# Performance work log

Measured on AMD Instinct MI355X. Metric: run time of the kernel, lower is better.

## Reference

```python
import jax, jax.numpy as jnp
import numpy as np
import math

N = 100000
D = 128       # input_dim
DK = 32       # d_k
H = 4         # heads
DV = D // H   # d_v = 32
DFF = 512     # 4 * input_dim
EPS = 1e-5


def layer_norm(x, g, b):
    mu = jnp.mean(x, axis=-1, keepdims=True)
    var = jnp.var(x, axis=-1, keepdims=True)
    return (x - mu) * jax.lax.rsqrt(var + EPS) * g + b


def setup_inputs() -> dict:
    key = jax.random.key(0)
    ks = jax.random.split(key, 10)
    x = jax.random.normal(ks[0], (N, D), dtype=jnp.float32)
    neighbor_index = jax.random.randint(ks[1], (N, 4), 0, N)
    # xavier-ish scaled params
    w_q = jax.random.normal(ks[2], (H, D, DK), dtype=jnp.float32) * math.sqrt(2.0 / (D + DK))
    w_k = jax.random.normal(ks[3], (H, 5, D, DK), dtype=jnp.float32) * math.sqrt(2.0 / (D + DK))
    w_v = jax.random.normal(ks[4], (H, 5, D, DV), dtype=jnp.float32) * math.sqrt(2.0 / (D + DV))
    W1 = jax.random.normal(ks[5], (D, DFF), dtype=jnp.float32) * math.sqrt(1.0 / D)
    b1 = jnp.zeros((DFF,), dtype=jnp.float32)
    W2 = jax.random.normal(ks[6], (DFF, D), dtype=jnp.float32) * math.sqrt(1.0 / DFF)
    b2 = jnp.zeros((D,), dtype=jnp.float32)
    g1 = jnp.ones((D,), dtype=jnp.float32)
    beta1 = jnp.zeros((D,), dtype=jnp.float32)
    g2 = jnp.ones((D,), dtype=jnp.float32)
    beta2 = jnp.zeros((D,), dtype=jnp.float32)
    return {"x": x, "neighbor_index": neighbor_index, "w_q": w_q, "w_k": w_k,
            "w_v": w_v, "W1": W1, "b1": b1, "W2": W2, "b2": b2,
            "g1": g1, "beta1": beta1, "g2": g2, "beta2": beta2}


def attention(x, neighbor_index, w_q, w_k, w_v):
    # gather the 4 typed neighbors and prepend the self node -> (N, 5, D)
    x_nb = jnp.concatenate([x[:, None, :], x[neighbor_index]], axis=1)
    Q = jnp.einsum('nd,hdk->hnk', x, w_q)                 # (H, N, DK)
    K = jnp.einsum('nrd,hrdk->hnrk', x_nb, w_k)           # (H, N, 5, DK)
    V = jnp.einsum('nrd,hrdv->hnrv', x_nb, w_v)           # (H, N, 5, DV)
    A = jnp.einsum('hnk,hnrk->hnr', Q, K) / math.sqrt(DK)
    # NOTE: original torch code applies softmax over dim=1 (the node axis),
    # reproduced faithfully here.
    A = jax.nn.softmax(A, axis=1)
    Z = jnp.einsum('hnr,hnrv->hnv', A, V)                 # (H, N, DV)
    return jnp.transpose(Z, (1, 0, 2)).reshape(x.shape[0], -1)  # (N, H*DV)


def reference(x, neighbor_index, w_q, w_k, w_v, W1, b1, W2, b2, g1, beta1, g2, beta2):
    attn = attention(x, neighbor_index, w_q, w_k, w_v)
    h = layer_norm(x + attn, g1, beta1)
    ffn = jax.nn.relu(h @ W1 + b1) @ W2 + b2
    return layer_norm(h + ffn, g2, beta2)
```

## Files before the change

kernel.cpp:

```cpp
#include <hip/hip_runtime.h>
#include <hip/hip_bf16.h>

typedef unsigned short u16;
typedef __attribute__((ext_vector_type(8))) short short8;
typedef __attribute__((ext_vector_type(4))) float f32x4;
typedef __attribute__((ext_vector_type(4))) float float4v;
typedef __attribute__((ext_vector_type(4))) unsigned short us4;
typedef __attribute__((ext_vector_type(4))) int int4v;

#define NN       100000
#define OFF_WK   16384
#define OFF_WV   98304
#define OFF_W1   180224
#define PACK_ELEMS 311296

#define WS_LWS   0u
#define WS_PM    8000000u
#define WS_PS    8000640u
#define WS_MHR   8001280u
#define WS_ISHR  8001408u
#define WS_PK    8001536u
#define WS_XB    8624128u
#define WS_SV    34224128u

#define PWS_PITCH 40
#define PWS_SLICE 1280

static __device__ __forceinline__ float b2f(u16 u){
  unsigned int i = ((unsigned int)u) << 16;
  float f; __builtin_memcpy(&f, &i, 4); return f;
}
static __device__ __forceinline__ u16 f2b(float f){
  unsigned int i; __builtin_memcpy(&i, &f, 4);
  i += 0x7FFFu + ((i >> 16) & 1u);
  return (u16)(i >> 16);
}
static __device__ __forceinline__ f32x4 mfma16(short8 a, short8 b, f32x4 c){
  return __builtin_amdgcn_mfma_f32_16x16x32_bf16(a, b, c, 0, 0, 0);
}
static __device__ __forceinline__ bool detect32(const void* g1){
  return ((const u16*)g1)[0] == 0;
}
static __device__ __forceinline__ float ldf(const void* p, size_t i, bool is32){
  return is32 ? ((const float*)p)[i] : b2f(((const u16*)p)[i]);
}

static __device__ __forceinline__ void stage16k(
    const u16* __restrict__ g, u16* l, int wv, int lane)
{
  #pragma unroll
  for (int k = 0; k < 4; k++){
    int off = wv*4096 + k*1024;
    __builtin_amdgcn_global_load_lds(
        (const __attribute__((address_space(1))) void*)((const char*)g + off + lane*16),
        (__attribute__((address_space(3))) void*)((char*)l + off),
        16, 0, 0);
  }
}

#define VMW4() asm volatile("s_waitcnt vmcnt(4)" ::: "memory")
#define VMW0() asm volatile("s_waitcnt vmcnt(0)" ::: "memory")
#define SBAR() asm volatile("s_barrier" ::: "memory")

__global__ __launch_bounds__(256) void k_convert_x(
    const void* __restrict__ x, const void* __restrict__ g1, u16* __restrict__ xb)
{
  const bool is32 = detect32(g1);
  size_t i = (size_t)blockIdx.x * 256 + threadIdx.x;
  us4 o;
  if (is32){
    float4v v = ((const float4v*)x)[i];
    o.x = f2b(v.x); o.y = f2b(v.y); o.z = f2b(v.z); o.w = f2b(v.w);
  } else {
    o = ((const us4*)x)[i];
  }
  ((us4*)xb)[i] = o;
}

__global__ __launch_bounds__(256) void k_pack(
    const void* __restrict__ wq, const void* __restrict__ wk,
    const void* __restrict__ wv, const void* __restrict__ W1,
    const void* __restrict__ W2, const void* __restrict__ g1,
    const void* __restrict__ b1, const void* __restrict__ b2,
    const void* __restrict__ be1, const void* __restrict__ g2,
    const void* __restrict__ be2,
    u16* __restrict__ pk, u16* __restrict__ sv)
{
  const bool is32 = detect32(g1);
  int p = blockIdx.x * 256 + threadIdx.x;
  if (p < PACK_ELEMS){
    float v;
    if (p < OFF_WK){
      int q = p;
      int j = q & 7, lane = (q >> 3) & 63, tk = q >> 9;
      int kb = tk & 3, t = tk >> 2;
      int kd = kb*32 + (lane>>4)*8 + j, nc = t*16 + (lane & 15);
      v = ldf(wq, (size_t)(nc>>5)*4096 + kd*32 + (nc & 31), is32);
    } else if (p < OFF_WV){
      int q = p - OFF_WK; int r = q >> 14; q &= 16383;
      int j = q & 7, lane = (q >> 3) & 63, tk = q >> 9;
      int kb = tk & 3, t = tk >> 2;
      int kd = kb*32 + (lane>>4)*8 + j, nc = t*16 + (lane & 15);
      v = ldf(wk, (size_t)((nc>>5)*5 + r)*4096 + kd*32 + (nc & 31), is32);
    } else if (p < OFF_W1){
      int q = p - OFF_WV; int r = q >> 14; q &= 16383;
      int j = q & 7, lane = (q >> 3) & 63, tk = q >> 9;
      int kb = tk & 3, t = tk >> 2;
      int kd = kb*32 + (lane>>4)*8 + j, nc = t*16 + (lane & 15);
      v = ldf(wv, (size_t)((nc>>5)*5 + r)*4096 + kd*32 + (nc & 31), is32);
    } else {
      int q = p - OFF_W1;
      int j = q & 7, lane = (q >> 3) & 63, rest = q >> 9;
      int pairIdx = rest >> 4, sub = rest & 15;
      int c = pairIdx >> 2, kb2 = pairIdx & 3;
      int half = lane >> 4, mc = lane & 15;
      if (sub < 8){
        int u = sub >> 2, kb = sub & 3;
        int kd = kb*32 + half*8 + j;
        int nc = c*128 + (kb2*2+u)*16 + mc;
        v = ldf(W1, (size_t)kd*512 + nc, is32);
      } else {
        int t = sub - 8;
        int kd = (c*4+kb2)*32 + half*8 + j;
        int nc = t*16 + mc;
        v = ldf(W2, (size_t)kd*128 + nc, is32);
      }
    }
    pk[p] = f2b(v);
  }
  if (blockIdx.x == 0){
    for (int i = threadIdx.x; i < 1152; i += 256){
      const void* src; int off;
      if      (i < 512) { src = b1;  off = i; }
      else if (i < 640) { src = b2;  off = i - 512; }
      else if (i < 768) { src = g1;  off = i - 640; }
      else if (i < 896) { src = be1; off = i - 768; }
      else if (i < 1024){ src = g2;  off = i - 896; }
      else              { src = be2; off = i - 1024; }
      sv[i] = f2b(ldf(src, off, is32));
    }
  }
}

__global__ __launch_bounds__(256, 4) void k_qk(
    const u16* __restrict__ x, const int* __restrict__ nbr,
    const u16* __restrict__ pw, float* __restrict__ lws)
{
  __shared__ __align__(16) u16 sbuf[16384];
  const int tid = threadIdx.x, lane = tid & 63, wv = tid >> 6;
  const int m = lane & 15, quad = lane >> 4;
  const int n0 = blockIdx.x * 128 + wv * 32;
  const bool act0 = (n0 < NN), act1 = (n0 + 16 < NN);
  const short8* sb8 = (const short8*)sbuf;

  int nd[2][4];
  short8 a2[2][4], a2n[2][4];
  #pragma unroll
  for (int tl = 0; tl < 2; tl++){
    if (!(tl ? act1 : act0)) continue;
    int4v t4 = *(const int4v*)(nbr + (size_t)(n0 + tl*16 + m)*4);
    nd[tl][0]=t4.x; nd[tl][1]=t4.y; nd[tl][2]=t4.z; nd[tl][3]=t4.w;
    const short8* xp = (const short8*)(x + (size_t)(n0 + tl*16 + m) * 128);
    #pragma unroll
    for (int kb = 0; kb < 4; kb++) a2[tl][kb] = xp[kb*4 + quad];
  }

  stage16k(pw, sbuf, wv, lane);
  stage16k(pw + 8192, sbuf + 8192, wv, lane);

  f32x4 q[2][8];
  #pragma unroll
  for (int tl = 0; tl < 2; tl++)
    #pragma unroll
    for (int t = 0; t < 8; t++) q[tl][t] = (f32x4){0.f,0.f,0.f,0.f};

  #pragma unroll
  for (int ph = 0; ph < 2; ph++){
    VMW4(); SBAR();
    const short8* cur = sb8 + (ph&1)*1024;
    #pragma unroll
    for (int tlc = 0; tlc < 4; tlc++){
      int t = ph*4 + tlc;
      short8 bfr[4];
      #pragma unroll
      for (int kb = 0; kb < 4; kb++) bfr[kb] = cur[(tlc*4+kb)*64 + lane];
      #pragma unroll
      for (int tl = 0; tl < 2; tl++){
        if (!(tl ? act1 : act0)) continue;
        #pragma unroll
        for (int kb = 0; kb < 4; kb++) q[tl][t] = mfma16(a2[tl][kb], bfr[kb], q[tl][t]);
      }
    }
    SBAR();
    stage16k(pw + OFF_WK + ph*8192, sbuf + (ph&1)*8192, wv, lane);
  }

  for (int r = 0; r < 5; r++){
    #pragma unroll
    for (int hf = 0; hf < 2; hf++){
      const int p = 2 + 2*r + hf;
      if (p < 11) { VMW4(); } else { VMW0(); }
      SBAR();
      const short8* cur = sb8 + (p&1)*1024;
      if (hf == 0 && r < 4){
        #pragma unroll
        for (int tl = 0; tl < 2; tl++){
          if (!(tl ? act1 : act0)) continue;
          const short8* gp = (const short8*)(x + (size_t)nd[tl][r] * 128);
          #pragma unroll
          for (int kb = 0; kb < 4; kb++) a2n[tl][kb] = gp[kb*4 + quad];
        }
      }
      #pragma unroll
      for (int hh = 0; hh < 2; hh++){
        const int h = hf*2 + hh;
        short8 b0[4], b1f[4];
        #pragma unroll
        for (int kb = 0; kb < 4; kb++){
          b0[kb]  = cur[((2*hh  )*4+kb)*64 + lane];
          b1f[kb] = cur[((2*hh+1)*4+kb)*64 + lane];
        }
        #pragma unroll
        for (int tl = 0; tl < 2; tl++){
          if (!(tl ? act1 : act0)) continue;
          f32x4 k0 = {0.f,0.f,0.f,0.f}, k1 = {0.f,0.f,0.f,0.f};
          #pragma unroll
          for (int kb = 0; kb < 4; kb++){
            k0 = mfma16(a2[tl][kb], b0[kb],  k0);
            k1 = mfma16(a2[tl][kb], b1f[kb], k1);
          }
          float pv[4];
          #pragma unroll
          for (int i = 0; i < 4; i++)
            pv[i] = q[tl][2*h][i]*k0[i] + q[tl][2*h+1][i]*k1[i];
          #pragma unroll
          for (int mask = 1; mask < 16; mask <<= 1){
            #pragma unroll
            for (int i = 0; i < 4; i++) pv[i] += __shfl_xor(pv[i], mask, 16);
          }
          if (m == 0){
            #pragma unroll
            for (int i = 0; i < 4; i++)
              lws[(size_t)(h*5+r)*NN + n0 + tl*16 + quad*4 + i]
                  = pv[i] * 0.17677669529663687f;
          }
        }
      }
      if (hf == 1 && r < 4){
        #pragma unroll
        for (int tl = 0; tl < 2; tl++)
          #pragma unroll
          for (int kb = 0; kb < 4; kb++) a2[tl][kb] = a2n[tl][kb];
      }
      SBAR();
      if (p <= 9)
        stage16k(pw + OFF_WK + (p+2-2)*8192, sbuf + (p&1)*8192, wv, lane);
    }
  }
}

__global__ __launch_bounds__(256) void k_red_part(
    const float* __restrict__ lws, float* __restrict__ pm, float* __restrict__ ps)
{
  const int hr = blockIdx.x >> 3, pb = blockIdx.x & 7;
  const int start = pb * 12500, end = start + 12500;
  const float* v = lws + (size_t)hr * NN;
  __shared__ float red[256];
  float mx = -1e30f;
  for (int i = start + threadIdx.x; i < end; i += 256) mx = fmaxf(mx, v[i]);
  red[threadIdx.x] = mx; __syncthreads();
  for (int s = 128; s > 0; s >>= 1){
    if ((int)threadIdx.x < s) red[threadIdx.x] = fmaxf(red[threadIdx.x], red[threadIdx.x+s]);
    __syncthreads();
  }
  mx = red[0]; __syncthreads();
  float sm = 0.f;
  for (int i = start + threadIdx.x; i < end; i += 256) sm += __expf(v[i] - mx);
  red[threadIdx.x] = sm; __syncthreads();
  for (int s = 128; s > 0; s >>= 1){
    if ((int)threadIdx.x < s) red[threadIdx.x] += red[threadIdx.x+s];
    __syncthreads();
  }
  if (threadIdx.x == 0){ pm[blockIdx.x] = mx; ps[blockIdx.x] = red[0]; }
}

__global__ __launch_bounds__(64) void k_red_fin(
    const float* __restrict__ pm, const float* __restrict__ ps,
    float* __restrict__ mhr, float* __restrict__ ishr)
{
  int t = threadIdx.x;
  if (t < 20){
    float M = -1e30f;
    for (int b = 0; b < 8; b++) M = fmaxf(M, pm[t*8+b]);
    float S = 0.f;
    for (int b = 0; b < 8; b++) S += ps[t*8+b] * __expf(pm[t*8+b] - M);
    mhr[t] = M; ishr[t] = 1.0f / S;
  }
}

__global__ __launch_bounds__(256, 3) void k_attn_ffn(
    const u16* __restrict__ x, const void* __restrict__ xraw,
    const int* __restrict__ nbr,
    const u16* __restrict__ pw, const float* __restrict__ lws,
    const float* __restrict__ mhr, const float* __restrict__ ishr,
    const u16* __restrict__ sv, const void* __restrict__ g1raw,
    float* __restrict__ out)
{
  __shared__ __align__(16) u16 sbuf[16384];
  __shared__ __align__(16) u16 upool[5120];
  const int tid = threadIdx.x, lane = tid & 63, wv = tid >> 6;
  const int m = lane & 15, quad = lane >> 4;
  const int n0 = blockIdx.x * 128 + wv * 32;
  const bool act0 = (n0 < NN), act1 = (n0 + 16 < NN);
  const bool is32 = detect32(g1raw);
  const u16* b1s = sv;
  const u16* b2s = sv + 512;
  const u16* g1s = sv + 640;
  const u16* be1s = sv + 768;
  const u16* g2s = sv + 896;
  const u16* be2s = sv + 1024;
  const short8* sb8 = (const short8*)sbuf;
  const u16* wvp = pw + OFF_WV;
  const u16* wfp = pw + OFF_W1;
  float* attw_w = ((float*)upool) + wv * 640;
  u16*   pws_w  = upool + wv * PWS_SLICE;

  for (int j = lane; j < 640; j += 64){
    int tl = j / 320, rem = j - tl*320;
    int r = rem >> 6, h = (rem >> 4) & 3, mm = rem & 15, hr = h*5 + r;
    int node = n0 + tl*16 + mm;
    attw_w[j] = (node < NN)
        ? __expf(lws[(size_t)hr*NN + node] - mhr[hr]) * ishr[hr] : 0.f;
  }

  int nd[2][4];
  short8 a2[2][4], a2n[2][4];
  #pragma unroll
  for (int tl = 0; tl < 2; tl++){
    if (!(tl ? act1 : act0)) continue;
    int4v t4 = *(const int4v*)(nbr + (size_t)(n0 + tl*16 + m)*4);
    nd[tl][0]=t4.x; nd[tl][1]=t4.y; nd[tl][2]=t4.z; nd[tl][3]=t4.w;
    const short8* xp = (const short8*)(x + (size_t)(n0 + tl*16 + m) * 128);
    #pragma unroll
    for (int kb = 0; kb < 4; kb++) a2[tl][kb] = xp[kb*4 + quad];
  }

  stage16k(wvp, sbuf, wv, lane);
  stage16k(wvp + 8192, sbuf + 8192, wv, lane);

  f32x4 zacc[2][8];
  #pragma unroll
  for (int tl = 0; tl < 2; tl++)
    #pragma unroll
    for (int t = 0; t < 8; t++) zacc[tl][t] = (f32x4){0.f,0.f,0.f,0.f};

  for (int r = 0; r < 5; r++){
    #pragma unroll
    for (int hf = 0; hf < 2; hf++){
      const int p = 2*r + hf;
      VMW4(); SBAR();
      const short8* cur = sb8 + (p&1)*1024;
      if (hf == 0 && r < 4){
        #pragma unroll
        for (int tl = 0; tl < 2; tl++){
          if (!(tl ? act1 : act0)) continue;
          const short8* gp = (const short8*)(x + (size_t)nd[tl][r] * 128);
          #pragma unroll
          for (int kb = 0; kb < 4; kb++) a2n[tl][kb] = gp[kb*4 + quad];
        }
      }
      #pragma unroll
      for (int tlc = 0; tlc < 4; tlc++){
        const int t = hf*4 + tlc;
        short8 bfr[4];
        #pragma unroll
        for (int kb = 0; kb < 4; kb++) bfr[kb] = cur[(tlc*4+kb)*64 + lane];
        const int h = t >> 1;
        #pragma unroll
        for (int tl = 0; tl < 2; tl++){
          if (!(tl ? act1 : act0)) continue;
          f32x4 v = {0.f,0.f,0.f,0.f};
          #pragma unroll
          for (int kb = 0; kb < 4; kb++) v = mfma16(a2[tl][kb], bfr[kb], v);
          const float* aw = attw_w + tl*320 + (r*4+h)*16;
          #pragma unroll
          for (int i = 0; i < 4; i++) zacc[tl][t][i] += aw[quad*4+i] * v[i];
        }
      }
      if (hf == 1 && r < 4){
        #pragma unroll
        for (int tl = 0; tl < 2; tl++)
          #pragma unroll
          for (int kb = 0; kb < 4; kb++) a2[tl][kb] = a2n[tl][kb];
      }
      SBAR();
      {
        const int b = p + 2;
        const u16* src = (b < 10) ? wvp + b*8192 : wfp + (b-10)*8192;
        stage16k(src, sbuf + (p&1)*8192, wv, lane);
      }
    }
  }

  float mu[2][4], rs[2][4];
  #pragma unroll
  for (int tl = 0; tl < 2; tl++){
    if (!(tl ? act1 : act0)) continue;
    int rowb = n0 + tl*16;
    #pragma unroll
    for (int t = 0; t < 8; t++)
      #pragma unroll
      for (int i = 0; i < 4; i++)
        zacc[tl][t][i] += ldf(xraw, (size_t)(rowb + quad*4 + i)*128 + t*16 + m, is32);
    float s1[4] = {0,0,0,0}, s2[4] = {0,0,0,0};
    #pragma unroll
    for (int t = 0; t < 8; t++)
      #pragma unroll
      for (int i = 0; i < 4; i++){ float y = zacc[tl][t][i]; s1[i] += y; s2[i] += y*y; }
    #pragma unroll
    for (int mask = 1; mask < 16; mask <<= 1){
      #pragma unroll
      for (int i = 0; i < 4; i++){
        s1[i] += __shfl_xor(s1[i], mask, 16);
        s2[i] += __shfl_xor(s2[i], mask, 16);
      }
    }
    #pragma unroll
    for (int i = 0; i < 4; i++){
      mu[tl][i] = s1[i] * (1.f/128.f);
      float var = s2[i] * (1.f/128.f) - mu[tl][i]*mu[tl][i];
      rs[tl][i] = rsqrtf(var + 1e-5f);
    }
  }

  unsigned int hDp[2][8][2];
  short8 ah[2][4];
  #pragma unroll
  for (int kb = 0; kb < 4; kb++){
    #pragma unroll
    for (int u = 0; u < 2; u++){
      int t = kb*2 + u;
      #pragma unroll
      for (int tl = 0; tl < 2; tl++){
        if (!(tl ? act1 : act0)) continue;
        float gg = b2f(g1s[t*16+m]), bb = b2f(be1s[t*16+m]);
        u16 hv[4];
        #pragma unroll
        for (int i = 0; i < 4; i++){
          hv[i] = f2b((zacc[tl][t][i]-mu[tl][i])*rs[tl][i]*gg + bb);
          pws_w[(tl*16 + quad*4 + i)*PWS_PITCH + u*16 + m] = hv[i];
        }
        hDp[tl][t][0] = (unsigned int)hv[0] | ((unsigned int)hv[1] << 16);
        hDp[tl][t][1] = (unsigned int)hv[2] | ((unsigned int)hv[3] << 16);
      }
    }
    #pragma unroll
    for (int tl = 0; tl < 2; tl++)
      ah[tl][kb] = *(const short8*)(pws_w + (tl*16 + m)*PWS_PITCH + quad*8);
  }

  f32x4 f2acc[2][8];
  #pragma unroll
  for (int tl = 0; tl < 2; tl++)
    #pragma unroll
    for (int t = 0; t < 8; t++) f2acc[tl][t] = (f32x4){0.f,0.f,0.f,0.f};

  for (int f = 0; f < 16; f++){
    const int p = 10 + f;
    if (p < 25) { VMW4(); } else { VMW0(); }
    SBAR();
    const short8* w1f = sb8 + (p&1)*1024;
    const short8* w2f = w1f + 512;
    const int c = f >> 2, kb2 = f & 3;
    #pragma unroll
    for (int u = 0; u < 2; u++){
      short8 bfr[4];
      #pragma unroll
      for (int kb = 0; kb < 4; kb++) bfr[kb] = w1f[(u*4+kb)*64 + lane];
      float b1c = b2f(b1s[c*128 + (kb2*2+u)*16 + m]);
      #pragma unroll
      for (int tl = 0; tl < 2; tl++){
        if (!(tl ? act1 : act0)) continue;
        f32x4 g = {0.f,0.f,0.f,0.f};
        #pragma unroll
        for (int kb = 0; kb < 4; kb++) g = mfma16(ah[tl][kb], bfr[kb], g);
        #pragma unroll
        for (int i = 0; i < 4; i++)
          pws_w[(tl*16 + quad*4 + i)*PWS_PITCH + u*16 + m]
              = f2b(fmaxf(g[i] + b1c, 0.f));
      }
    }
    short8 ag[2];
    #pragma unroll
    for (int tl = 0; tl < 2; tl++)
      ag[tl] = *(const short8*)(pws_w + (tl*16 + m)*PWS_PITCH + quad*8);
    #pragma unroll
    for (int t = 0; t < 8; t++){
      short8 bf = w2f[t*64 + lane];
      #pragma unroll
      for (int tl = 0; tl < 2; tl++){
        if (!(tl ? act1 : act0)) continue;
        f2acc[tl][t] = mfma16(ag[tl], bf, f2acc[tl][t]);
      }
    }
    SBAR();
    if (p <= 23)
      stage16k(wfp + (f+2)*8192, sbuf + (p&1)*8192, wv, lane);
  }

  #pragma unroll
  for (int tl = 0; tl < 2; tl++){
    if (!(tl ? act1 : act0)) continue;
    int rowb = n0 + tl*16;
    #pragma unroll
    for (int t = 0; t < 8; t++){
      float b2c = b2f(b2s[t*16 + m]);
      f2acc[tl][t][0] += b2f((u16)(hDp[tl][t][0] & 0xffff)) + b2c;
      f2acc[tl][t][1] += b2f((u16)(hDp[tl][t][0] >> 16))    + b2c;
      f2acc[tl][t][2] += b2f((u16)(hDp[tl][t][1] & 0xffff)) + b2c;
      f2acc[tl][t][3] += b2f((u16)(hDp[tl][t][1] >> 16))    + b2c;
    }
    float s1[4] = {0,0,0,0}, s2[4] = {0,0,0,0};
    #pragma unroll
    for (int t = 0; t < 8; t++)
      #pragma unroll
      for (int i = 0; i < 4; i++){ float y = f2acc[tl][t][i]; s1[i] += y; s2[i] += y*y; }
    #pragma unroll
    for (int mask = 1; mask < 16; mask <<= 1){
      #pragma unroll
      for (int i = 0; i < 4; i++){
        s1[i] += __shfl_xor(s1[i], mask, 16);
        s2[i] += __shfl_xor(s2[i], mask, 16);
      }
    }
    float mu2[4], rs2[4];
    #pragma unroll
    for (int i = 0; i < 4; i++){
      mu2[i] = s1[i] * (1.f/128.f);
      float var = s2[i] * (1.f/128.f) - mu2[i]*mu2[i];
      rs2[i] = rsqrtf(var + 1e-5f);
    }
    #pragma unroll
    for (int t = 0; t < 8; t++){
      float gg = b2f(g2s[t*16+m]), bb = b2f(be2s[t*16+m]);
      #pragma unroll
      for (int i = 0; i < 4; i++)
        out[(size_t)(rowb + quad*4 + i)*128 + t*16 + m] =
            (f2acc[tl][t][i]-mu2[i])*rs2[i]*gg + bb;
    }
  }
}

extern "C" void kernel_launch(void* const* d_in, const int* in_sizes, int n_in,
                              void* d_out, int out_size, void* d_ws, size_t ws_size,
                              hipStream_t stream)
{
  const void* x   = d_in[0];
  const int*  nbr = (const int*)d_in[1];
  const void* wq  = d_in[2];
  const void* wk  = d_in[3];
  const void* wv  = d_in[4];
  const void* W1  = d_in[5];
  const void* b1  = d_in[6];
  const void* W2  = d_in[7];
  const void* b2  = d_in[8];
  const void* g1  = d_in[9];
  const void* be1 = d_in[10];
  const void* g2  = d_in[11];
  const void* be2 = d_in[12];
  float* out = (float*)d_out;

  char* ws = (char*)d_ws;
  float* lws  = (float*)(ws + WS_LWS);
  float* pm   = (float*)(ws + WS_PM);
  float* ps   = (float*)(ws + WS_PS);
  float* mhr  = (float*)(ws + WS_MHR);
  float* ishr = (float*)(ws + WS_ISHR);
  u16*   pk   = (u16*)  (ws + WS_PK);
  u16*   xb   = (u16*)  (ws + WS_XB);
  u16*   sv   = (u16*)  (ws + WS_SV);

  k_convert_x<<<dim3(12500), dim3(256), 0, stream>>>(x, g1, xb);
  k_pack<<<dim3((PACK_ELEMS+255)/256), dim3(256), 0, stream>>>(wq, wk, wv, W1, W2, g1,
                                                               b1, b2, be1, g2, be2, pk, sv);
  k_qk<<<dim3((NN+127)/128), dim3(256), 0, stream>>>(xb, nbr, pk, lws);
  k_red_part<<<dim3(160), dim3(256), 0, stream>>>(lws, pm, ps);
  k_red_fin<<<dim3(1), dim3(64), 0, stream>>>(pm, ps, mhr, ishr);
  k_attn_ffn<<<dim3((NN+127)/128), dim3(256), 0, stream>>>(xb, x, nbr, pk, lws, mhr, ishr,
                                                           sv, g1, out);
}
```

Before: 350.8 us.

## Fuse prep kernels, fold softmax finalize, swizzle workgroups, add MFMA priority

```diff
diff --git a/kernel.cpp b/kernel.cpp
--- a/kernel.cpp
+++ b/kernel.cpp
@@ -9,6 +9,7 @@
 typedef __attribute__((ext_vector_type(4))) int int4v;
 
 #define NN       100000
+#define NWG      782
 #define OFF_WK   16384
 #define OFF_WV   98304
 #define OFF_W1   180224
@@ -17,14 +18,12 @@
 #define WS_LWS   0u
 #define WS_PM    8000000u
 #define WS_PS    8000640u
-#define WS_MHR   8001280u
-#define WS_ISHR  8001408u
 #define WS_PK    8001536u
 #define WS_XB    8624128u
 #define WS_SV    34224128u
 
 #define PWS_PITCH 40
-#define PWS_SLICE 1280
+#define PWS_SLICE 640
 
 static __device__ __forceinline__ float b2f(u16 u){
   unsigned int i = ((unsigned int)u) << 16;
@@ -43,6 +42,11 @@
 }
 static __device__ __forceinline__ float ldf(const void* p, size_t i, bool is32){
   return is32 ? ((const float*)p)[i] : b2f(((const u16*)p)[i]);
+}
+static __device__ __forceinline__ int swz_wg(int b){
+  const int q = NWG >> 3, r = NWG & 7;
+  int x = b & 7, i = b >> 3;
+  return (x < r ? x*(q+1) : r*(q+1) + (x-r)*q) + i;
 }
 
 static __device__ __forceinline__ void stage16k(
@@ -61,32 +65,30 @@
 #define VMW4() asm volatile("s_waitcnt vmcnt(4)" ::: "memory")
 #define VMW0() asm volatile("s_waitcnt vmcnt(0)" ::: "memory")
 #define SBAR() asm volatile("s_barrier" ::: "memory")
-
-__global__ __launch_bounds__(256) void k_convert_x(
-    const void* __restrict__ x, const void* __restrict__ g1, u16* __restrict__ xb)
+#define PRIO1() __builtin_amdgcn_s_setprio(1)
+#define PRIO0() __builtin_amdgcn_s_setprio(0)
+
+__global__ __launch_bounds__(256) void k_prep(
+    const void* __restrict__ x, const void* __restrict__ wq,
+    const void* __restrict__ wk, const void* __restrict__ wv,
+    const void* __restrict__ W1, const void* __restrict__ W2,
+    const void* __restrict__ g1, const void* __restrict__ b1,
+    const void* __restrict__ b2, const void* __restrict__ be1,
+    const void* __restrict__ g2, const void* __restrict__ be2,
+    u16* __restrict__ xb, u16* __restrict__ pk, u16* __restrict__ sv)
 {
   const bool is32 = detect32(g1);
-  size_t i = (size_t)blockIdx.x * 256 + threadIdx.x;
-  us4 o;
-  if (is32){
-    float4v v = ((const float4v*)x)[i];
-    o.x = f2b(v.x); o.y = f2b(v.y); o.z = f2b(v.z); o.w = f2b(v.w);
-  } else {
-    o = ((const us4*)x)[i];
-  }
-  ((us4*)xb)[i] = o;
-}
-
-__global__ __launch_bounds__(256) void k_pack(
-    const void* __restrict__ wq, const void* __restrict__ wk,
-    const void* __restrict__ wv, const void* __restrict__ W1,
-    const void* __restrict__ W2, const void* __restrict__ g1,
-    const void* __restrict__ b1, const void* __restrict__ b2,
-    const void* __restrict__ be1, const void* __restrict__ g2,
-    const void* __restrict__ be2,
-    u16* __restrict__ pk, u16* __restrict__ sv)
-{
-  const bool is32 = detect32(g1);
+  {
+    size_t i = (size_t)blockIdx.x * 256 + threadIdx.x;
+    us4 o;
+    if (is32){
+      float4v v = ((const float4v*)x)[i];
+      o.x = f2b(v.x); o.y = f2b(v.y); o.z = f2b(v.z); o.w = f2b(v.w);
+    } else {
+      o = ((const us4*)x)[i];
+    }
+    ((us4*)xb)[i] = o;
+  }
   int p = blockIdx.x * 256 + threadIdx.x;
   if (p < PACK_ELEMS){
     float v;
@@ -142,14 +144,15 @@
   }
 }
 
-__global__ __launch_bounds__(256, 4) void k_qk(
+__global__ __launch_bounds__(256) void k_qk(
     const u16* __restrict__ x, const int* __restrict__ nbr,
     const u16* __restrict__ pw, float* __restrict__ lws)
 {
   __shared__ __align__(16) u16 sbuf[16384];
   const int tid = threadIdx.x, lane = tid & 63, wv = tid >> 6;
   const int m = lane & 15, quad = lane >> 4;
-  const int n0 = blockIdx.x * 128 + wv * 32;
+  const int blk = swz_wg(blockIdx.x);
+  const int n0 = blk * 128 + wv * 32;
   const bool act0 = (n0 < NN), act1 = (n0 + 16 < NN);
   const short8* sb8 = (const short8*)sbuf;
 
@@ -178,6 +181,7 @@
   for (int ph = 0; ph < 2; ph++){
     VMW4(); SBAR();
     const short8* cur = sb8 + (ph&1)*1024;
+    PRIO1();
     #pragma unroll
     for (int tlc = 0; tlc < 4; tlc++){
       int t = ph*4 + tlc;
@@ -191,6 +195,7 @@
         for (int kb = 0; kb < 4; kb++) q[tl][t] = mfma16(a2[tl][kb], bfr[kb], q[tl][t]);
       }
     }
+    PRIO0();
     SBAR();
     stage16k(pw + OFF_WK + ph*8192, sbuf + (ph&1)*8192, wv, lane);
   }
@@ -224,11 +229,13 @@
         for (int tl = 0; tl < 2; tl++){
           if (!(tl ? act1 : act0)) continue;
           f32x4 k0 = {0.f,0.f,0.f,0.f}, k1 = {0.f,0.f,0.f,0.f};
+          PRIO1();
           #pragma unroll
           for (int kb = 0; kb < 4; kb++){
             k0 = mfma16(a2[tl][kb], b0[kb],  k0);
             k1 = mfma16(a2[tl][kb], b1f[kb], k1);
           }
+          PRIO0();
           float pv[4];
           #pragma unroll
           for (int i = 0; i < 4; i++)
@@ -254,7 +261,7 @@
       }
       SBAR();
       if (p <= 9)
-        stage16k(pw + OFF_WK + (p+2-2)*8192, sbuf + (p&1)*8192, wv, lane);
+        stage16k(pw + OFF_WK + p*8192, sbuf + (p&1)*8192, wv, lane);
     }
   }
 }
@@ -284,33 +291,20 @@
   if (threadIdx.x == 0){ pm[blockIdx.x] = mx; ps[blockIdx.x] = red[0]; }
 }
 
-__global__ __launch_bounds__(64) void k_red_fin(
-    const float* __restrict__ pm, const float* __restrict__ ps,
-    float* __restrict__ mhr, float* __restrict__ ishr)
-{
-  int t = threadIdx.x;
-  if (t < 20){
-    float M = -1e30f;
-    for (int b = 0; b < 8; b++) M = fmaxf(M, pm[t*8+b]);
-    float S = 0.f;
-    for (int b = 0; b < 8; b++) S += ps[t*8+b] * __expf(pm[t*8+b] - M);
-    mhr[t] = M; ishr[t] = 1.0f / S;
-  }
-}
-
-__global__ __launch_bounds__(256, 3) void k_attn_ffn(
+__global__ __launch_bounds__(256) void k_attn_ffn(
     const u16* __restrict__ x, const void* __restrict__ xraw,
     const int* __restrict__ nbr,
     const u16* __restrict__ pw, const float* __restrict__ lws,
-    const float* __restrict__ mhr, const float* __restrict__ ishr,
+    const float* __restrict__ pm, const float* __restrict__ ps,
     const u16* __restrict__ sv, const void* __restrict__ g1raw,
     float* __restrict__ out)
 {
   __shared__ __align__(16) u16 sbuf[16384];
-  __shared__ __align__(16) u16 upool[5120];
+  __shared__ __align__(16) u16 upool[2560];
   const int tid = threadIdx.x, lane = tid & 63, wv = tid >> 6;
   const int m = lane & 15, quad = lane >> 4;
-  const int n0 = blockIdx.x * 128 + wv * 32;
+  const int blk = swz_wg(blockIdx.x);
+  const int n0 = blk * 128 + wv * 32;
   const bool act0 = (n0 < NN), act1 = (n0 + 16 < NN);
   const bool is32 = detect32(g1raw);
   const u16* b1s = sv;
@@ -322,15 +316,27 @@
   const short8* sb8 = (const short8*)sbuf;
   const u16* wvp = pw + OFF_WV;
   const u16* wfp = pw + OFF_W1;
-  float* attw_w = ((float*)upool) + wv * 640;
-  u16*   pws_w  = upool + wv * PWS_SLICE;
+  u16* attw_w = upool + wv * PWS_SLICE;
+  u16* pws_w  = upool + wv * PWS_SLICE;
+
+  float Mreg = -1e30f, iSreg = 0.f;
+  if (lane < 20){
+    float M = -1e30f;
+    #pragma unroll
+    for (int b = 0; b < 8; b++) M = fmaxf(M, pm[lane*8+b]);
+    float S = 0.f;
+    #pragma unroll
+    for (int b = 0; b < 8; b++) S += ps[lane*8+b] * __expf(pm[lane*8+b] - M);
+    Mreg = M; iSreg = 1.0f / S;
+  }
 
   for (int j = lane; j < 640; j += 64){
     int tl = j / 320, rem = j - tl*320;
     int r = rem >> 6, h = (rem >> 4) & 3, mm = rem & 15, hr = h*5 + r;
     int node = n0 + tl*16 + mm;
+    float Mh = __shfl(Mreg, hr), iSh = __shfl(iSreg, hr);
     attw_w[j] = (node < NN)
-        ? __expf(lws[(size_t)hr*NN + node] - mhr[hr]) * ishr[hr] : 0.f;
+        ? f2b(__expf(lws[(size_t)hr*NN + node] - Mh) * iSh) : (u16)0;
   }
 
   int nd[2][4];
@@ -380,11 +386,13 @@
         for (int tl = 0; tl < 2; tl++){
           if (!(tl ? act1 : act0)) continue;
           f32x4 v = {0.f,0.f,0.f,0.f};
+          PRIO1();
           #pragma unroll
           for (int kb = 0; kb < 4; kb++) v = mfma16(a2[tl][kb], bfr[kb], v);
-          const float* aw = attw_w + tl*320 + (r*4+h)*16;
-          #pragma unroll
-          for (int i = 0; i < 4; i++) zacc[tl][t][i] += aw[quad*4+i] * v[i];
+          PRIO0();
+          const u16* aw = attw_w + tl*320 + (r*4+h)*16;
+          #pragma unroll
+          for (int i = 0; i < 4; i++) zacc[tl][t][i] += b2f(aw[quad*4+i]) * v[i];
         }
       }
       if (hf == 1 && r < 4){
@@ -436,27 +444,25 @@
   unsigned int hDp[2][8][2];
   short8 ah[2][4];
   #pragma unroll
-  for (int kb = 0; kb < 4; kb++){
-    #pragma unroll
-    for (int u = 0; u < 2; u++){
-      int t = kb*2 + u;
-      #pragma unroll
-      for (int tl = 0; tl < 2; tl++){
-        if (!(tl ? act1 : act0)) continue;
+  for (int tl = 0; tl < 2; tl++){
+    if (!(tl ? act1 : act0)) continue;
+    #pragma unroll
+    for (int kb = 0; kb < 4; kb++){
+      #pragma unroll
+      for (int u = 0; u < 2; u++){
+        int t = kb*2 + u;
         float gg = b2f(g1s[t*16+m]), bb = b2f(be1s[t*16+m]);
         u16 hv[4];
         #pragma unroll
         for (int i = 0; i < 4; i++){
           hv[i] = f2b((zacc[tl][t][i]-mu[tl][i])*rs[tl][i]*gg + bb);
-          pws_w[(tl*16 + quad*4 + i)*PWS_PITCH + u*16 + m] = hv[i];
+          pws_w[(quad*4 + i)*PWS_PITCH + u*16 + m] = hv[i];
         }
         hDp[tl][t][0] = (unsigned int)hv[0] | ((unsigned int)hv[1] << 16);
         hDp[tl][t][1] = (unsigned int)hv[2] | ((unsigned int)hv[3] << 16);
       }
-    }
-    #pragma unroll
-    for (int tl = 0; tl < 2; tl++)
-      ah[tl][kb] = *(const short8*)(pws_w + (tl*16 + m)*PWS_PITCH + quad*8);
+      ah[tl][kb] = *(const short8*)(pws_w + m*PWS_PITCH + quad*8);
+    }
   }
 
   f32x4 f2acc[2][8];
@@ -472,28 +478,29 @@
     const short8* w1f = sb8 + (p&1)*1024;
     const short8* w2f = w1f + 512;
     const int c = f >> 2, kb2 = f & 3;
-    #pragma unroll
-    for (int u = 0; u < 2; u++){
-      short8 bfr[4];
-      #pragma unroll
-      for (int kb = 0; kb < 4; kb++) bfr[kb] = w1f[(u*4+kb)*64 + lane];
-      float b1c = b2f(b1s[c*128 + (kb2*2+u)*16 + m]);
-      #pragma unroll
-      for (int tl = 0; tl < 2; tl++){
-        if (!(tl ? act1 : act0)) continue;
+    short8 ag[2];
+    #pragma unroll
+    for (int tl = 0; tl < 2; tl++){
+      if (!(tl ? act1 : act0)) continue;
+      #pragma unroll
+      for (int u = 0; u < 2; u++){
+        short8 bfr[4];
+        #pragma unroll
+        for (int kb = 0; kb < 4; kb++) bfr[kb] = w1f[(u*4+kb)*64 + lane];
+        float b1c = b2f(b1s[c*128 + (kb2*2+u)*16 + m]);
         f32x4 g = {0.f,0.f,0.f,0.f};
+        PRIO1();
         #pragma unroll
         for (int kb = 0; kb < 4; kb++) g = mfma16(ah[tl][kb], bfr[kb], g);
+        PRIO0();
         #pragma unroll
         for (int i = 0; i < 4; i++)
-          pws_w[(tl*16 + quad*4 + i)*PWS_PITCH + u*16 + m]
+          pws_w[(quad*4 + i)*PWS_PITCH + u*16 + m]
               = f2b(fmaxf(g[i] + b1c, 0.f));
       }
-    }
-    short8 ag[2];
-    #pragma unroll
-    for (int tl = 0; tl < 2; tl++)
-      ag[tl] = *(const short8*)(pws_w + (tl*16 + m)*PWS_PITCH + quad*8);
+      ag[tl] = *(const short8*)(pws_w + m*PWS_PITCH + quad*8);
+    }
+    PRIO1();
     #pragma unroll
     for (int t = 0; t < 8; t++){
       short8 bf = w2f[t*64 + lane];
@@ -503,6 +510,7 @@
         f2acc[tl][t] = mfma16(ag[tl], bf, f2acc[tl][t]);
       }
     }
+    PRIO0();
     SBAR();
     if (p <= 23)
       stage16k(wfp + (f+2)*8192, sbuf + (p&1)*8192, wv, lane);
@@ -574,18 +582,14 @@
   float* lws  = (float*)(ws + WS_LWS);
   float* pm   = (float*)(ws + WS_PM);
   float* ps   = (float*)(ws + WS_PS);
-  float* mhr  = (float*)(ws + WS_MHR);
-  float* ishr = (float*)(ws + WS_ISHR);
   u16*   pk   = (u16*)  (ws + WS_PK);
   u16*   xb   = (u16*)  (ws + WS_XB);
   u16*   sv   = (u16*)  (ws + WS_SV);
 
-  k_convert_x<<<dim3(12500), dim3(256), 0, stream>>>(x, g1, xb);
-  k_pack<<<dim3((PACK_ELEMS+255)/256), dim3(256), 0, stream>>>(wq, wk, wv, W1, W2, g1,
-                                                               b1, b2, be1, g2, be2, pk, sv);
-  k_qk<<<dim3((NN+127)/128), dim3(256), 0, stream>>>(xb, nbr, pk, lws);
+  k_prep<<<dim3(12500), dim3(256), 0, stream>>>(x, wq, wk, wv, W1, W2, g1,
+                                                b1, b2, be1, g2, be2, xb, pk, sv);
+  k_qk<<<dim3(NWG), dim3(256), 0, stream>>>(xb, nbr, pk, lws);
   k_red_part<<<dim3(160), dim3(256), 0, stream>>>(lws, pm, ps);
-  k_red_fin<<<dim3(1), dim3(64), 0, stream>>>(pm, ps, mhr, ishr);
-  k_attn_ffn<<<dim3((NN+127)/128), dim3(256), 0, stream>>>(xb, x, nbr, pk, lws, mhr, ishr,
-                                                           sv, g1, out);
-}
+  k_attn_ffn<<<dim3(NWG), dim3(256), 0, stream>>>(xb, x, nbr, pk, lws, pm, ps,
+                                                  sv, g1, out);
+}
```

Result: slower. 402.6 us (+14.8%).
